# Kernel tuning notes

Measured on AMD Instinct MI355X. Metric: run time of the kernel, lower is better.

Reference implementation:

```python
import jax, jax.numpy as jnp
import numpy as np

N = 20000
F_IN = 500
HID = 64
CLS = 16
H = 4
K_KNN = 10
NEG_SLOPE = 0.2


def _edges(key, n_rand):
    # random edges plus self-loops (mirrors add_self_loops in the torch code)
    src = jax.random.randint(key, (n_rand,), 0, N)
    dst = jax.random.randint(jax.random.fold_in(key, 1), (n_rand,), 0, N)
    loops = jnp.arange(N)
    return jnp.stack([jnp.concatenate([src, loops]), jnp.concatenate([dst, loops])]).astype(jnp.int32)


def setup_inputs():
    key = jax.random.key(0)
    ks = jax.random.split(key, 40)
    inp = {}
    inp['x'] = jax.random.normal(ks[0], (N, F_IN), jnp.float32)
    inp['edge_index_1'] = _edges(ks[1], 16 * N)          # 1-hop graph, 340k edges
    inp['edge_index_2'] = _edges(ks[2], 32 * N)          # denser 2-hop graph, 660k edges
    knn_src = jnp.repeat(jnp.arange(N), K_KNN)
    knn_dst = jax.random.randint(ks[3], (K_KNN * N,), 0, N)
    inp['edge_index_knn'] = jnp.stack([knn_src, knn_dst]).astype(jnp.int32)

    def p(k, shape):
        return jax.random.normal(k, shape, jnp.float32) * 0.05

    dims = {1: (F_IN, HID), 2: (HID, CLS), 3: (F_IN, HID), 4: (HID, CLS), 5: (F_IN, HID), 6: (HID, CLS)}
    i = 4
    for j in range(1, 7):
        fi, fo = dims[j]
        inp[f'W{j}'] = p(ks[i], (fi, H, fo)); i += 1
        inp[f'as{j}'] = p(ks[i], (H, fo)); i += 1
        inp[f'ad{j}'] = p(ks[i], (H, fo)); i += 1
        inp[f'b{j}'] = jnp.zeros((fo,), jnp.float32)
    for j in range(1, 4):
        inp[f'lin{j}_w'] = p(ks[i], (CLS, CLS)); i += 1
        inp[f'lin{j}_b'] = jnp.zeros((CLS,), jnp.float32)
    inp['agg_w'] = p(ks[i], (CLS,))
    return inp


def gat_conv(x, ei, W, a_s, a_d, b):
    # PyG GATConv, concat=False (mean over heads). W: [F,H,D], a_s/a_d: [H,D], b: [D]
    src, dst = ei[0], ei[1]
    z = jnp.einsum('nf,fhd->nhd', x, W)                 # [N,H,D]
    e_src = jnp.sum(z * a_s, -1)                         # [N,H]
    e_dst = jnp.sum(z * a_d, -1)                         # [N,H]
    e = jax.nn.leaky_relu(e_src[src] + e_dst[dst], NEG_SLOPE)   # [E,H]
    m = jax.ops.segment_max(e, dst, num_segments=N)      # per-dst softmax (edge softmax)
    p = jnp.exp(e - m[dst])
    s = jax.ops.segment_sum(p, dst, num_segments=N)
    alpha = p / (s[dst] + 1e-16)                         # [E,H]
    out = jax.ops.segment_sum(alpha[:, :, None] * z[src], dst, num_segments=N)  # [N,H,D]
    return out.mean(1) + b


def reference(x, edge_index_1, edge_index_2, edge_index_knn,
              W1, as1, ad1, b1, W2, as2, ad2, b2,
              W3, as3, ad3, b3, W4, as4, ad4, b4,
              W5, as5, ad5, b5, W6, as6, ad6, b6,
              lin1_w, lin1_b, lin2_w, lin2_b, lin3_w, lin3_b, agg_w):
    # eval mode: dropout is a no-op
    h1 = jax.nn.relu(gat_conv(x, edge_index_1, W1, as1, ad1, b1))
    h1 = gat_conv(h1, edge_index_1, W2, as2, ad2, b2)
    h2 = jax.nn.relu(gat_conv(x, edge_index_2, W3, as3, ad3, b3))
    h2 = gat_conv(h2, edge_index_2, W4, as4, ad4, b4)
    h3 = jax.nn.relu(gat_conv(x, edge_index_knn, W5, as5, ad5, b5))
    h3 = gat_conv(h3, edge_index_knn, W6, as6, ad6, b6)

    a1 = jnp.tanh(h1 @ lin1_w + lin1_b) @ agg_w          # [N]
    a2 = jnp.tanh(h2 @ lin2_w + lin2_b) @ agg_w
    a3 = jnp.tanh(h3 @ lin3_w + lin3_b) @ agg_w
    a = jax.nn.softmax(jnp.stack([a1, a2, a3], axis=1), axis=1)  # [N,3]
    h = a[:, 0:1] * h1 + a[:, 1:2] * h2 + a[:, 2:3] * h3
    return jax.nn.log_softmax(h, axis=1)
```

## Files before the change

### kernel.cpp

```cpp
#include <hip/hip_runtime.h>
#include <hip/hip_bf16.h>
#include <math.h>

#define N_NODES 20000
#define MP      20096
#define FIN     500
#define KP      512
#define NBUCK   157

typedef unsigned short u16;
typedef unsigned char  u8;
typedef __attribute__((ext_vector_type(8))) short   short8;
typedef __attribute__((ext_vector_type(2))) unsigned uv2;
typedef __attribute__((ext_vector_type(2))) float   f32x2;
typedef __attribute__((ext_vector_type(4))) float   f32x4;

__device__ __forceinline__ float b2f(u16 u){
  union { unsigned int i; float f; } v; v.i = ((unsigned int)u) << 16; return v.f;
}
__device__ __forceinline__ u16 f2b(float f){
  __hip_bfloat16 h = __float2bfloat16(f);
  return *reinterpret_cast<u16*>(&h);
}
__device__ __forceinline__ float lrelu(float x){ return x >= 0.f ? x : 0.2f * x; }
__device__ __forceinline__ float ldp(const void* p, int i, int bf){
  return bf ? b2f(((const u16*)p)[i]) : ((const float*)p)[i];
}
__device__ __forceinline__ u8 f2fp8(float f){
  return (u8)(__builtin_amdgcn_cvt_pk_fp8_f32(f, 0.f, 0, false) & 0xff);
}
template<bool HI>
__device__ __forceinline__ f32x2 fp8pair(unsigned w){
  return __builtin_amdgcn_cvt_pk_f32_fp8((int)w, HI);
}
__device__ __forceinline__ void gll16(const u16* g, u16* l){
  __builtin_amdgcn_global_load_lds(
      (const __attribute__((address_space(1))) unsigned int*)g,
      (__attribute__((address_space(3))) unsigned int*)l, 16, 0, 0);
}
__device__ __forceinline__ void barrier_lgkm(){
  asm volatile("s_waitcnt lgkmcnt(0)" ::: "memory");
  __builtin_amdgcn_s_barrier();
  asm volatile("" ::: "memory");
}
__device__ __forceinline__ float ftanh(float x){
  float ex = __expf(2.f * x);
  return 1.f - 2.f / (ex + 1.f);
}

__global__ __launch_bounds__(1024) void detect_dtype_kernel(const unsigned int* __restrict__ xw, int nwords,
                                                            int* __restrict__ flag){
  __shared__ int cnt;
  if (threadIdx.x == 0) cnt = 0;
  __syncthreads();
  int c = 0;
  for (int i = threadIdx.x; i < nwords; i += 1024){
    unsigned e = (xw[i] >> 7) & 0xFF;
    if (e >= 0x70 && e <= 0x8F) c++;
  }
  atomicAdd(&cnt, c);
  __syncthreads();
  if (threadIdx.x == 0) *flag = (cnt * 2 > nwords) ? 1 : 0;
}

#define CHA 8192
#define PB  1024
__global__ __launch_bounds__(PB) void prep_kernel(
    const void* __restrict__ x, u16* __restrict__ xp,
    const void* Wb0, const void* Wb1, const void* Wb2,
    const void* Ws0, const void* Ws1, const void* Ws2,
    u16* ob0, u16* ob1, u16* ob2, u16* os0, u16* os1, u16* os2,
    const int* s0, const int* s1, const int* s2,
    const int* d0, const int* d1, const int* d2,
    int E0, int E1, int E2, int S0, int S1, int S2, int EB,
    int* __restrict__ bucketCur, unsigned* p0, unsigned* p1, unsigned* p2,
    const int* __restrict__ flag){
  __shared__ int hb[NBUCK];
  __shared__ int loff[NBUCK];
  __shared__ int hbase[NBUCK];
  __shared__ unsigned shp[CHA];
  __shared__ u8 shb[CHA];
  __shared__ u16 tile[64][65];
  int bf = *flag;
  int tid = threadIdx.x;
  if (blockIdx.y == 0){
    int t = blockIdx.x * PB + tid;
    if (t >= MP * 64) return;
    int row = t >> 6;
    int j0  = (t & 63) * 8;
    short8 v = {0,0,0,0,0,0,0,0};
    if (row < N_NODES){
      if (j0 + 8 <= FIN){
        if (bf){
          const ushort4* xr = (const ushort4*)((const u16*)x + (size_t)row * FIN + j0);
          ushort4 a = xr[0], b = xr[1];
          v[0]=(short)a.x; v[1]=(short)a.y; v[2]=(short)a.z; v[3]=(short)a.w;
          v[4]=(short)b.x; v[5]=(short)b.y; v[6]=(short)b.z; v[7]=(short)b.w;
        } else {
          const float4* xr = (const float4*)((const float*)x + (size_t)row * FIN + j0);
          float4 a = xr[0], b = xr[1];
          v[0]=(short)f2b(a.x); v[1]=(short)f2b(a.y); v[2]=(short)f2b(a.z); v[3]=(short)f2b(a.w);
          v[4]=(short)f2b(b.x); v[5]=(short)f2b(b.y); v[6]=(short)f2b(b.z); v[7]=(short)f2b(b.w);
        }
      } else {
#pragma unroll
        for (int j = 0; j < 8; ++j){
          int k = j0 + j;
          u16 val = 0;
          if (k < FIN)
            val = bf ? ((const u16*)x)[(size_t)row * FIN + k]
                     : f2b(((const float*)x)[(size_t)row * FIN + k]);
          v[j] = (short)val;
        }
      }
    }
    *(short8*)(xp + (size_t)row * KP + j0) = v;
  } else if (blockIdx.y == 1){
    int xb = blockIdx.x;
    if (xb >= 96 + 3) return;
    int tx = tid & 63, tyb = tid >> 6;
    const void* Wsrc; u16* O; int SRCW, SRCH, DSTW, kt, nt;
    if (xb < 96){
      int which = xb >> 5, tl = xb & 31;
      nt = (tl & 3) << 6; kt = (tl >> 2) << 6;
      Wsrc = which == 0 ? Wb0 : (which == 1 ? Wb1 : Wb2);
      O    = which == 0 ? ob0 : (which == 1 ? ob1 : ob2);
      SRCW = 256; SRCH = FIN; DSTW = KP;
    } else {
      int which = xb - 96;
      nt = 0; kt = 0;
      Wsrc = which == 0 ? Ws0 : (which == 1 ? Ws1 : Ws2);
      O    = which == 0 ? os0 : (which == 1 ? os1 : os2);
      SRCW = 64; SRCH = 64; DSTW = 64;
    }
#pragma unroll
    for (int r = 0; r < 4; ++r){
      int kl = tyb + r * 16;
      int k = kt + kl, n = nt + tx;
      u16 vv = 0;
      if (k < SRCH)
        vv = bf ? ((const u16*)Wsrc)[(size_t)k * SRCW + n]
                : f2b(((const float*)Wsrc)[(size_t)k * SRCW + n]);
      tile[kl][tx] = vv;
    }
    __syncthreads();
#pragma unroll
    for (int r = 0; r < 4; ++r){
      int nl = tyb + r * 16;
      O[(size_t)(nt + nl) * DSTW + kt + tx] = tile[tx][nl];
    }
  } else {
    int sblk = blockIdx.x;
    if (sblk >= 3 * EB) return;
    int g = sblk / EB;
    const int* src = g == 0 ? s0 : (g == 1 ? s1 : s2);
    const int* dst = g == 0 ? d0 : (g == 1 ? d1 : d2);
    unsigned* pairs = g == 0 ? p0 : (g == 1 ? p1 : p2);
    int E = g == 0 ? E0 : (g == 1 ? E1 : E2);
    int S = g == 0 ? S0 : (g == 1 ? S1 : S2);
    int base = (sblk % EB) * CHA;
    if (base >= E) return;
    if (tid < NBUCK) hb[tid] = 0;
    __syncthreads();
    constexpr int EPT = CHA / PB;
    int rk[EPT]; unsigned pr[EPT]; int bk[EPT]; bool vl[EPT];
#pragma unroll
    for (int i = 0; i < EPT; ++i){
      int e = base + i * PB + tid;
      vl[i] = e < E;
      bk[i] = 0; rk[i] = 0; pr[i] = 0;
      if (vl[i]){
        int dd = dst[e], ss = src[e];
        bk[i] = dd >> 7;
        pr[i] = ((unsigned)ss << 7) | (unsigned)(dd & 127);
        rk[i] = atomicAdd(&hb[bk[i]], 1);
      }
    }
    __syncthreads();
    int ret = 0;
    if (tid < NBUCK) ret = atomicAdd(&bucketCur[g * NBUCK + tid], hb[tid]);
    if (tid == 0){
      int run = 0;
      for (int k = 0; k < NBUCK; ++k){ loff[k] = run; run += hb[k]; }
    }
    barrier_lgkm();
#pragma unroll
    for (int i = 0; i < EPT; ++i)
      if (vl[i]){
        int j = loff[bk[i]] + rk[i];
        shp[j] = pr[i];
        shb[j] = (u8)bk[i];
      }
    if (tid < NBUCK) hbase[tid] = ret;
    __syncthreads();
    int nb = E - base; if (nb > CHA) nb = CHA;
    for (int j = tid; j < nb; j += PB){
      int b = shb[j];
      int pos = hbase[b] + (j - loff[b]);
      if (pos < S)
        pairs[(size_t)b * S + pos] = shp[j];
    }
  }
}

__global__ __launch_bounds__(256) void gemm_big_kernel(const u16* __restrict__ A,
    const u16* B0, const u16* B1, const u16* B2,
    u8* C0, u8* C1, u8* C2,
    const void* as0, const void* as1, const void* as2,
    const void* ad0, const void* ad1, const void* ad2,
    float* __restrict__ esB, float* __restrict__ edB,
    const int* __restrict__ flag, int M,
    const unsigned* p0, const unsigned* p1, const unsigned* p2,
    int S0, int S1, int S2, const int* __restrict__ bucketCur,
    int* e0, int* e1, int* e2, int2* __restrict__ metaB){
  __shared__ alignas(16) u16 As[128 * 64];
  __shared__ alignas(16) u16 Bs[128 * 64];
  __shared__ int ccnt[128];
  __shared__ int cloff[128];
  __shared__ int ccur[128];
  int t = threadIdx.x;
  if (blockIdx.z == 1){
    int bxc = blockIdx.x;
    if (bxc >= 3 * NBUCK) return;
    int g = bxc / NBUCK, b = bxc - g * NBUCK;
    const unsigned* pairs = g == 0 ? p0 : (g == 1 ? p1 : p2);
    int* esrc = g == 0 ? e0 : (g == 1 ? e1 : e2);
    int S = g == 0 ? S0 : (g == 1 ? S1 : S2);
    int2* meta = metaB + (size_t)g * MP;
    int nb = bucketCur[g * NBUCK + b];
    if (nb > S) nb = S;
    const unsigned* pb = pairs + (size_t)b * S;
    int* eb = esrc + (size_t)b * S;
    if (t < 128) ccnt[t] = 0;
    __syncthreads();
    for (int i = t; i < nb; i += 256)
      atomicAdd(&ccnt[pb[i] & 127], 1);
    __syncthreads();
    if (t == 0){
      int run = 0;
      for (int k = 0; k < 128; ++k){ cloff[k] = run; run += ccnt[k]; }
    }
    __syncthreads();
    if (t < 128){
      ccur[t] = cloff[t];
      int d = b * 128 + t;
      if (d < N_NODES){
        int2 m; m.x = b * S + cloff[t]; m.y = ccnt[t];
        meta[d] = m;
      }
    }
    __syncthreads();
    for (int i = t; i < nb; i += 256){
      unsigned u = pb[i];
      int slot = atomicAdd(&ccur[u & 127], 1);
      eb[slot] = (int)(u >> 7);
    }
    return;
  }
  int bx = blockIdx.x;
  int grp = bx / 48, j = bx - grp * 48;
  int ng = j >> 3, sub = j & 7;
  int mt = grp * 8 + sub;
  if (mt >= MP / 128) return;
  int g  = ng >> 1;
  int n0 = (ng & 1) * 128;
  int m0 = mt * 128;
  const u16* BT = g == 0 ? B0 : (g == 1 ? B1 : B2);
  u8* C = g == 0 ? C0 : (g == 1 ? C1 : C2);
  const void* as_ = g == 0 ? as0 : (g == 1 ? as1 : as2);
  const void* ad_ = g == 0 ? ad0 : (g == 1 ? ad1 : ad2);
  float* es = esB + (size_t)g * N_NODES * 4;
  float* ed = edB + (size_t)g * N_NODES * 4;
  const int K = KP, Nn = 256;
  int lane = t & 63, w = t >> 6;
  int mw = (w >> 1) * 64, nw = (w & 1) * 64;
  f32x4 acc[4][4] = {};
  for (int k0 = 0; k0 < K; k0 += 64){
    __syncthreads();
#pragma unroll
    for (int i = 0; i < 4; ++i){
      int c = i * 256 + w * 64 + lane;
      int row = c >> 3, slot = c & 7;
      int kk = ((slot ^ (row & 7))) * 8;
      gll16(A  + (size_t)(m0 + row) * K + k0 + kk, As + (size_t)(i * 256 + w * 64) * 8);
      gll16(BT + (size_t)(n0 + row) * K + k0 + kk, Bs + (size_t)(i * 256 + w * 64) * 8);
    }
    __syncthreads();
#pragma unroll
    for (int ks = 0; ks < 2; ++ks){
      short8 af[4], bfr[4];
#pragma unroll
      for (int mi = 0; mi < 4; ++mi){
        int row = mw + mi * 16 + (lane & 15);
        int sl = (ks * 4 + (lane >> 4)) ^ (row & 7);
        af[mi] = *(const short8*)(As + (size_t)row * 64 + sl * 8);
      }
#pragma unroll
      for (int ni = 0; ni < 4; ++ni){
        int row = nw + ni * 16 + (lane & 15);
        int sl = (ks * 4 + (lane >> 4)) ^ (row & 7);
        bfr[ni] = *(const short8*)(Bs + (size_t)row * 64 + sl * 8);
      }
#pragma unroll
      for (int mi = 0; mi < 4; ++mi)
#pragma unroll
        for (int ni = 0; ni < 4; ++ni)
          acc[mi][ni] = __builtin_amdgcn_mfma_f32_16x16x32_bf16(af[mi], bfr[ni], acc[mi][ni], 0, 0, 0);
    }
  }
  int bf = *flag;
#pragma unroll
  for (int mi = 0; mi < 4; ++mi)
#pragma unroll
    for (int ni = 0; ni < 4; ++ni)
#pragma unroll
      for (int r = 0; r < 4; ++r){
        int row = m0 + mw + mi * 16 + (lane >> 4) * 4 + r;
        int col = n0 + nw + ni * 16 + (lane & 15);
        if (row < M) C[(size_t)row * Nn + col] = f2fp8(acc[mi][ni][r]);
      }
  {
    int h = (n0 + nw) >> 6;
    float asv[4], adv[4];
#pragma unroll
    for (int ni = 0; ni < 4; ++ni){
      int col = n0 + nw + ni * 16 + (lane & 15);
      asv[ni] = ldp(as_, col, bf);
      adv[ni] = ldp(ad_, col, bf);
    }
#pragma unroll
    for (int mi = 0; mi < 4; ++mi)
#pragma unroll
      for (int r = 0; r < 4; ++r){
        float ps = 0.f, pd2 = 0.f;
#pragma unroll
        for (int ni = 0; ni < 4; ++ni){
          ps  += acc[mi][ni][r] * asv[ni];
          pd2 += acc[mi][ni][r] * adv[ni];
        }
#pragma unroll
        for (int m2 = 1; m2 < 16; m2 <<= 1){
          ps  += __shfl_xor(ps, m2);
          pd2 += __shfl_xor(pd2, m2);
        }
        int row = m0 + mw + mi * 16 + (lane >> 4) * 4 + r;
        if ((lane & 15) == 0 && row < M){
          es[(size_t)row * 4 + h] = ps;
          ed[(size_t)row * 4 + h] = pd2;
        }
      }
  }
}

__global__ __launch_bounds__(256) void gemm_small_kernel(
    const u16* A0, const u16* A1, const u16* A2,
    const u16* B0, const u16* B1, const u16* B2,
    u8* C0, u8* C1, u8* C2,
    const void* as0, const void* as1, const void* as2,
    const void* ad0, const void* ad1, const void* ad2,
    float* __restrict__ esB, float* __restrict__ edB,
    const int* __restrict__ flag, int M){
  int g = blockIdx.y;
  const u16* A  = g == 0 ? A0 : (g == 1 ? A1 : A2);
  const u16* BT = g == 0 ? B0 : (g == 1 ? B1 : B2);
  u8* C = g == 0 ? C0 : (g == 1 ? C1 : C2);
  const void* as_ = g == 0 ? as0 : (g == 1 ? as1 : as2);
  const void* ad_ = g == 0 ? ad0 : (g == 1 ? ad1 : ad2);
  float* es = esB + (size_t)g * N_NODES * 4;
  float* ed = edB + (size_t)g * N_NODES * 4;
  __shared__ alignas(16) u16 As[64 * 64];
  __shared__ alignas(16) u16 Bs[64 * 64];
  int t = threadIdx.x, lane = t & 63, w = t >> 6;
  int m0 = blockIdx.x * 64;
#pragma unroll
  for (int i = 0; i < 2; ++i){
    int c = i * 256 + w * 64 + lane;
    int row = c >> 3, slot = c & 7;
    int kk = ((slot ^ (row & 7))) * 8;
    gll16(A  + (size_t)(m0 + row) * 64 + kk, As + (size_t)(i * 256 + w * 64) * 8);
    gll16(BT + (size_t)row * 64 + kk,        Bs + (size_t)(i * 256 + w * 64) * 8);
  }
  __syncthreads();
  f32x4 acc[4] = {};
  int mw = w * 16;
#pragma unroll
  for (int ks = 0; ks < 2; ++ks){
    int rowa = mw + (lane & 15);
    int sla = (ks * 4 + (lane >> 4)) ^ (rowa & 7);
    short8 af = *(const short8*)(As + (size_t)rowa * 64 + sla * 8);
#pragma unroll
    for (int ni = 0; ni < 4; ++ni){
      int rowb = ni * 16 + (lane & 15);
      int slb = (ks * 4 + (lane >> 4)) ^ (rowb & 7);
      short8 bv = *(const short8*)(Bs + (size_t)rowb * 64 + slb * 8);
      acc[ni] = __builtin_amdgcn_mfma_f32_16x16x32_bf16(af, bv, acc[ni], 0, 0, 0);
    }
  }
  int bf = *flag;
#pragma unroll
  for (int ni = 0; ni < 4; ++ni)
#pragma unroll
    for (int r = 0; r < 4; ++r){
      int row = m0 + mw + (lane >> 4) * 4 + r;
      int col = ni * 16 + (lane & 15);
      if (row < M) C[(size_t)row * 64 + col] = f2fp8(acc[ni][r]);
    }
  {
    float asv[4], adv[4];
#pragma unroll
    for (int ni = 0; ni < 4; ++ni){
      int col = ni * 16 + (lane & 15);
      asv[ni] = ldp(as_, col, bf);
      adv[ni] = ldp(ad_, col, bf);
    }
#pragma unroll
    for (int r = 0; r < 4; ++r){
      float ps[4], pd2[4];
#pragma unroll
      for (int ni = 0; ni < 4; ++ni){ ps[ni] = acc[ni][r] * asv[ni]; pd2[ni] = acc[ni][r] * adv[ni]; }
#pragma unroll
      for (int m2 = 1; m2 < 16; m2 <<= 1)
#pragma unroll
        for (int ni = 0; ni < 4; ++ni){
          ps[ni]  += __shfl_xor(ps[ni], m2);
          pd2[ni] += __shfl_xor(pd2[ni], m2);
        }
      int row = m0 + mw + (lane >> 4) * 4 + r;
      if ((lane & 15) == 0 && row < M){
#pragma unroll
        for (int ni = 0; ni < 4; ++ni){
          es[(size_t)row * 4 + ni] = ps[ni];
          ed[(size_t)row * 4 + ni] = pd2[ni];
        }
      }
    }
  }
}

template<int DT, bool RELU, bool BF16OUT, int PIPE>
__global__ __launch_bounds__(256) void gat_agg5_kernel(
    const u8* z0, const u8* z1, const u8* z2,
    const float* __restrict__ esB, const float* __restrict__ edB,
    const int2* __restrict__ metaB,
    const int* e0p, const int* e1p, const int* e2p,
    const void* b0, const void* b1, const void* b2,
    void* o0, void* o1, void* o2,
    const int* __restrict__ flag){
  int g = blockIdx.y;
  const u8* z = g == 0 ? z0 : (g == 1 ? z1 : z2);
  const int* esrc = g == 0 ? e0p : (g == 1 ? e1p : e2p);
  const void* bias = g == 0 ? b0 : (g == 1 ? b1 : b2);
  void* out = g == 0 ? o0 : (g == 1 ? o1 : o2);
  const float* es = esB + (size_t)g * N_NODES * 4;
  const float* ed = edB + (size_t)g * N_NODES * 4;
  const int2* meta = metaB + (size_t)g * MP;
  int bf = *flag;

  int d = (blockIdx.x * 256 + threadIdx.x) >> 6;
  int lane = threadIdx.x & 63;
  if (d >= N_NODES) return;
  constexpr int LPG = DT / 8;
  constexpr int G   = 64 / LPG;
  constexpr int HD  = DT / 4;
  int grp = lane / LPG;
  int li  = lane % LPG;
  int c0  = li * 8;
  int h   = c0 / HD;

  int2 md = meta[d];
  int deg = md.y;
  const int* ep = esrc + md.x;
  float edh = ed[(unsigned)d * 4 + h];

  float acc[8] = {0,0,0,0,0,0,0,0};
  float sacc = 0.f;

  int steps = (deg + PIPE * G - 1) / (PIPE * G);
  for (int tb = 0; tb < steps; ++tb){
    int e0 = tb * PIPE * G + grp;
    int s[PIPE]; float q[PIPE]; uv2 v[PIPE]; bool val[PIPE];
#pragma unroll
    for (int i = 0; i < PIPE; ++i){
      int e = e0 + i * G;
      val[i] = e < deg;
      int sl = ep[e];
      s[i] = val[i] ? sl : 0;
    }
#pragma unroll
    for (int i = 0; i < PIPE; ++i) q[i] = es[(unsigned)s[i] * 4 + h];
#pragma unroll
    for (int i = 0; i < PIPE; ++i) v[i] = *(const uv2*)(z + (unsigned)s[i] * DT + c0);
#pragma unroll
    for (int i = 0; i < PIPE; ++i){
      float p = val[i] ? __expf(lrelu(q[i] + edh)) : 0.f;
      sacc += p;
      f32x2 a0 = fp8pair<false>(v[i][0]), a1 = fp8pair<true>(v[i][0]);
      f32x2 a2 = fp8pair<false>(v[i][1]), a3 = fp8pair<true>(v[i][1]);
      acc[0] = fmaf(p, a0.x, acc[0]); acc[1] = fmaf(p, a0.y, acc[1]);
      acc[2] = fmaf(p, a1.x, acc[2]); acc[3] = fmaf(p, a1.y, acc[3]);
      acc[4] = fmaf(p, a2.x, acc[4]); acc[5] = fmaf(p, a2.y, acc[5]);
      acc[6] = fmaf(p, a3.x, acc[6]); acc[7] = fmaf(p, a3.y, acc[7]);
    }
  }

#pragma unroll
  for (int m = LPG; m < 64; m <<= 1){
    sacc += __shfl_xor(sacc, m);
#pragma unroll
    for (int j = 0; j < 8; ++j) acc[j] += __shfl_xor(acc[j], m);
  }
  float inv = 1.f / (sacc + 1e-16f);
  float v8[8];
#pragma unroll
  for (int j = 0; j < 8; ++j) v8[j] = acc[j] * inv;
#pragma unroll
  for (int m = HD / 8; m < LPG; m <<= 1)
#pragma unroll
    for (int j = 0; j < 8; ++j) v8[j] += __shfl_xor(v8[j], m);

  if (lane < HD / 8){
    if constexpr (BF16OUT){
      short8 ov;
#pragma unroll
      for (int j = 0; j < 8; ++j){
        float o = v8[j] * 0.25f + ldp(bias, lane * 8 + j, bf);
        if (RELU) o = fmaxf(o, 0.f);
        ov[j] = (short)f2b(o);
      }
      *(short8*)((u16*)out + (size_t)d * HD + lane * 8) = ov;
    } else {
      float o[8];
#pragma unroll
      for (int j = 0; j < 8; ++j){
        o[j] = v8[j] * 0.25f + ldp(bias, lane * 8 + j, bf);
        if (RELU) o[j] = fmaxf(o[j], 0.f);
      }
      float* op = (float*)out + (size_t)d * HD + lane * 8;
      *(float4*)op = make_float4(o[0], o[1], o[2], o[3]);
      *(float4*)(op + 4) = make_float4(o[4], o[5], o[6], o[7]);
    }
  }
}

__global__ __launch_bounds__(256) void final_combine_kernel(
    const float* __restrict__ h1, const float* __restrict__ h2, const float* __restrict__ h3,
    const void* l1w, const void* l1b, const void* l2w, const void* l2b,
    const void* l3w, const void* l3b, const void* aggw,
    void* __restrict__ outv, int n, const int* __restrict__ flag){
  __shared__ float Lw[3][16][16];
  __shared__ float Lb[3][16];
  __shared__ float Ag[16];
  int t = threadIdx.x;
  int bf = *flag;
  {
    const void* ws[3] = { l1w, l2w, l3w };
    for (int g = 0; g < 3; ++g) Lw[g][t / 16][t % 16] = ldp(ws[g], t, bf);
    if (t < 16){
      Lb[0][t] = ldp(l1b, t, bf); Lb[1][t] = ldp(l2b, t, bf); Lb[2][t] = ldp(l3b, t, bf);
      Ag[t] = ldp(aggw, t, bf);
    }
  }
  __syncthreads();
  int node = blockIdx.x * 256 + t;
  if (node >= n) return;
  const float* hp[3] = { h1, h2, h3 };
  float hv[3][16];
  float a[3];
  for (int g = 0; g < 3; ++g){
    const float4* h4 = (const float4*)(hp[g] + (size_t)node * 16);
#pragma unroll
    for (int q = 0; q < 4; ++q){
      float4 f = h4[q];
      hv[g][q * 4 + 0] = f.x; hv[g][q * 4 + 1] = f.y;
      hv[g][q * 4 + 2] = f.z; hv[g][q * 4 + 3] = f.w;
    }
    float dot = 0.f;
#pragma unroll
    for (int j = 0; j < 16; ++j){
      float acc2 = Lb[g][j];
#pragma unroll
      for (int i = 0; i < 16; ++i) acc2 += hv[g][i] * Lw[g][i][j];
      dot += ftanh(acc2) * Ag[j];
    }
    a[g] = dot;
  }
  float am = fmaxf(a[0], fmaxf(a[1], a[2]));
  float e0 = __expf(a[0] - am), e1 = __expf(a[1] - am), e2 = __expf(a[2] - am);
  float einv = 1.f / (e0 + e1 + e2);
  float w0 = e0 * einv, w1 = e1 * einv, w2 = e2 * einv;
  float hh[16];
  float hmax = -INFINITY;
#pragma unroll
  for (int i = 0; i < 16; ++i){
    hh[i] = w0 * hv[0][i] + w1 * hv[1][i] + w2 * hv[2][i];
    hmax = fmaxf(hmax, hh[i]);
  }
  float se = 0.f;
#pragma unroll
  for (int i = 0; i < 16; ++i) se += __expf(hh[i] - hmax);
  float ls = hmax + logf(se);
#pragma unroll
  for (int i = 0; i < 16; ++i){
    float o = hh[i] - ls;
    if (bf) ((__hip_bfloat16*)outv)[(size_t)node * 16 + i] = __float2bfloat16(o);
    else    ((float*)outv)[(size_t)node * 16 + i] = o;
  }
}

extern "C" void kernel_launch(void* const* d_in, const int* in_sizes, int n_in,
                              void* d_out, int out_size, void* d_ws, size_t ws_size,
                              hipStream_t stream){
  const void* x = d_in[0];
  const int* ei[3] = { (const int*)d_in[1], (const int*)d_in[2], (const int*)d_in[3] };
  int E[3] = { in_sizes[1] / 2, in_sizes[2] / 2, in_sizes[3] / 2 };
  int Emax = E[0] > E[1] ? E[0] : E[1]; if (E[2] > Emax) Emax = E[2];
  int EB = (Emax + CHA - 1) / CHA;
  int S[3];
  for (int g = 0; g < 3; ++g){
    long s = ((long)E[g] * 27 / 20) / NBUCK + 64;
    s &= ~63L; if (s > 8192) s = 8192;
    S[g] = (int)s;
  }
  const void *W[6], *as_[6], *ad_[6], *bb[6];
  for (int j = 0; j < 6; ++j){
    W[j]   = d_in[4 + 4 * j];
    as_[j] = d_in[5 + 4 * j];
    ad_[j] = d_in[6 + 4 * j];
    bb[j]  = d_in[7 + 4 * j];
  }
  const void* l1w = d_in[28]; const void* l1b = d_in[29];
  const void* l2w = d_in[30]; const void* l2b = d_in[31];
  const void* l3w = d_in[32]; const void* l3b = d_in[33];
  const void* agg = d_in[34];

  char* p = (char*)d_ws;
  auto alloc = [&](size_t bytes) -> void* {
    void* r = (void*)p;
    p += (bytes + 255) & ~(size_t)255;
    return r;
  };
  int* dflag = (int*)alloc(256);
  u16* xp = (u16*)alloc((size_t)MP * KP * 2);
  u16* hmid[3]; for (int g = 0; g < 3; ++g) hmid[g] = xp + (size_t)g * MP * 64;
  u16* wtb[3]; for (int g = 0; g < 3; ++g) wtb[g] = (u16*)alloc((size_t)256 * KP * 2);
  u16* wts[3]; for (int g = 0; g < 3; ++g) wts[g] = (u16*)alloc((size_t)64 * 64 * 2);
  u8* zf[3];   for (int g = 0; g < 3; ++g) zf[g]  = (u8*)alloc((size_t)N_NODES * 256 + 256);
  float* hbr[3]; for (int g = 0; g < 3; ++g) hbr[g] = (float*)alloc((size_t)N_NODES * 16 * 4);
  float* esB = (float*)alloc((size_t)3 * N_NODES * 4 * 4);
  float* edB = (float*)alloc((size_t)3 * N_NODES * 4 * 4);
  int* bucketCur = (int*)alloc((size_t)3 * NBUCK * 4);
  int2* metaB    = (int2*)alloc((size_t)3 * MP * 8);
  int* esrc[3];
  for (int g = 0; g < 3; ++g) esrc[g] = (int*)alloc(((size_t)NBUCK * S[g] + 256) * 4);
  unsigned* pairs[3];
  for (int g = 0; g < 3; ++g) pairs[g] = (unsigned*)alloc(((size_t)NBUCK * S[g] + 256) * 4);

  const int* s0 = ei[0];          const int* s1 = ei[1];          const int* s2 = ei[2];
  const int* d0 = ei[0] + E[0];   const int* d1 = ei[1] + E[1];   const int* d2 = ei[2] + E[2];

  (void)hipMemsetAsync(bucketCur, 0, (size_t)3 * NBUCK * 4, stream);
  detect_dtype_kernel<<<1, 1024, 0, stream>>>((const unsigned int*)x, 4096, dflag);
  prep_kernel<<<dim3((MP * 64 + PB - 1) / PB, 3), PB, 0, stream>>>(
      x, xp, W[0], W[2], W[4], W[1], W[3], W[5],
      wtb[0], wtb[1], wtb[2], wts[0], wts[1], wts[2],
      s0, s1, s2, d0, d1, d2, E[0], E[1], E[2], S[0], S[1], S[2], EB,
      bucketCur, pairs[0], pairs[1], pairs[2], dflag);

  const int convGrid = (N_NODES + 3) / 4;

  gemm_big_kernel<<<dim3(20 * 48, 1, 2), 256, 0, stream>>>(
      xp, wtb[0], wtb[1], wtb[2], zf[0], zf[1], zf[2],
      as_[0], as_[2], as_[4], ad_[0], ad_[2], ad_[4], esB, edB, dflag, N_NODES,
      pairs[0], pairs[1], pairs[2], S[0], S[1], S[2], bucketCur,
      esrc[0], esrc[1], esrc[2], metaB);
  gat_agg5_kernel<256, true, true, 6><<<dim3(convGrid, 3), 256, 0, stream>>>(
      zf[0], zf[1], zf[2], esB, edB, metaB, esrc[0], esrc[1], esrc[2],
      bb[0], bb[2], bb[4], (void*)hmid[0], (void*)hmid[1], (void*)hmid[2], dflag);

  gemm_small_kernel<<<dim3(MP / 64, 3), 256, 0, stream>>>(
      hmid[0], hmid[1], hmid[2], wts[0], wts[1], wts[2], zf[0], zf[1], zf[2],
      as_[1], as_[3], as_[5], ad_[1], ad_[3], ad_[5], esB, edB, dflag, N_NODES);
  gat_agg5_kernel<64, false, false, 4><<<dim3(convGrid, 3), 256, 0, stream>>>(
      zf[0], zf[1], zf[2], esB, edB, metaB, esrc[0], esrc[1], esrc[2],
      bb[1], bb[3], bb[5], (void*)hbr[0], (void*)hbr[1], (void*)hbr[2], dflag);

  final_combine_kernel<<<(N_NODES + 255) / 256, 256, 0, stream>>>(
      hbr[0], hbr[1], hbr[2], l1w, l1b, l2w, l2b, l3w, l3b, agg,
      d_out, N_NODES, dflag);
}
```

Before: 323.7 us.

## Compute edge softmax weights once per edge-head and broadcast via shuffles

```diff
diff --git a/kernel.cpp b/kernel.cpp
--- a/kernel.cpp
+++ b/kernel.cpp
@@ -462,44 +462,65 @@
   constexpr int LPG = DT / 8;
   constexpr int G   = 64 / LPG;
   constexpr int HD  = DT / 4;
+  constexpr int CHK = PIPE * G;
+  constexpr int TBS = 64 / CHK;
+  constexpr int BULK = TBS * CHK;
   int grp = lane / LPG;
   int li  = lane % LPG;
   int c0  = li * 8;
   int h   = c0 / HD;
+  int gh4 = (grp << 2) | h;
+  int ebk = lane >> 2;
+  int hbk = lane & 3;
 
   int2 md = meta[d];
   int deg = md.y;
   const int* ep = esrc + md.x;
-  float edh = ed[(unsigned)d * 4 + h];
+  const u8* zl = z + c0;
+  float edhb = ed[(unsigned)d * 4 + hbk];
 
   float acc[8] = {0,0,0,0,0,0,0,0};
   float sacc = 0.f;
 
-  int steps = (deg + PIPE * G - 1) / (PIPE * G);
-  for (int tb = 0; tb < steps; ++tb){
-    int e0 = tb * PIPE * G + grp;
-    int s[PIPE]; float q[PIPE]; uv2 v[PIPE]; bool val[PIPE];
-#pragma unroll
-    for (int i = 0; i < PIPE; ++i){
-      int e = e0 + i * G;
-      val[i] = e < deg;
-      int sl = ep[e];
-      s[i] = val[i] ? sl : 0;
-    }
-#pragma unroll
-    for (int i = 0; i < PIPE; ++i) q[i] = es[(unsigned)s[i] * 4 + h];
-#pragma unroll
-    for (int i = 0; i < PIPE; ++i) v[i] = *(const uv2*)(z + (unsigned)s[i] * DT + c0);
-#pragma unroll
-    for (int i = 0; i < PIPE; ++i){
-      float p = val[i] ? __expf(lrelu(q[i] + edh)) : 0.f;
-      sacc += p;
-      f32x2 a0 = fp8pair<false>(v[i][0]), a1 = fp8pair<true>(v[i][0]);
-      f32x2 a2 = fp8pair<false>(v[i][1]), a3 = fp8pair<true>(v[i][1]);
-      acc[0] = fmaf(p, a0.x, acc[0]); acc[1] = fmaf(p, a0.y, acc[1]);
-      acc[2] = fmaf(p, a1.x, acc[2]); acc[3] = fmaf(p, a1.y, acc[3]);
-      acc[4] = fmaf(p, a2.x, acc[4]); acc[5] = fmaf(p, a2.y, acc[5]);
-      acc[6] = fmaf(p, a3.x, acc[6]); acc[7] = fmaf(p, a3.y, acc[7]);
+  for (int base = 0; base < deg; base += BULK){
+    int nloc = deg - base; if (nloc > BULK) nloc = BULK;
+    int eid = 0;
+    if (lane < nloc) eid = ep[base + lane];
+    float pb[4];
+#pragma unroll
+    for (int j = 0; j < 4; ++j){
+      pb[j] = 0.f;
+      if (j * 16 < nloc){
+        int sl = j * 16 + ebk;
+        int pe = __shfl(eid, sl);
+        float ev = es[(unsigned)pe * 4 + hbk];
+        float pv = __expf(lrelu(ev + edhb));
+        pb[j] = (sl < nloc) ? pv : 0.f;
+      }
+    }
+#pragma unroll
+    for (int tb = 0; tb < TBS; ++tb){
+      if (tb * CHK >= nloc) break;
+      int s_[PIPE]; float q_[PIPE]; uv2 v_[PIPE];
+#pragma unroll
+      for (int i = 0; i < PIPE; ++i){
+        int sb = tb * CHK + i * G;
+        s_[i] = __shfl(eid, sb + grp);
+        q_[i] = __shfl(pb[sb >> 4], ((sb & 15) << 2) + gh4);
+      }
+#pragma unroll
+      for (int i = 0; i < PIPE; ++i) v_[i] = *(const uv2*)(zl + (unsigned)s_[i] * DT);
+#pragma unroll
+      for (int i = 0; i < PIPE; ++i){
+        float p = q_[i];
+        sacc += p;
+        f32x2 a0 = fp8pair<false>(v_[i][0]), a1 = fp8pair<true>(v_[i][0]);
+        f32x2 a2 = fp8pair<false>(v_[i][1]), a3 = fp8pair<true>(v_[i][1]);
+        acc[0] = fmaf(p, a0.x, acc[0]); acc[1] = fmaf(p, a0.y, acc[1]);
+        acc[2] = fmaf(p, a1.x, acc[2]); acc[3] = fmaf(p, a1.y, acc[3]);
+        acc[4] = fmaf(p, a2.x, acc[4]); acc[5] = fmaf(p, a2.y, acc[5]);
+        acc[6] = fmaf(p, a3.x, acc[6]); acc[7] = fmaf(p, a3.y, acc[7]);
+      }
     }
   }
 
```

Result: slower. 370.7 us (+14.5%).
